# Optimization experiments

Measured on AMD Instinct MI355X. Metric: run time of the kernel, lower is better.

The kernel has to match this reference:

```python
import jax, jax.numpy as jnp
import numpy as np

BETA, ALPHA, NS_STEPS = 0.9, 1.0, 1
D_MODEL, D_STATE, D_CONV, EXPAND = 768, 16, 4, 2
D_INNER = EXPAND * D_MODEL
DT_RANK = -(-D_MODEL // 16)  # ceil(d_model/16) = 48
B, L = 2, 1024


def setup_inputs() -> dict:
    key = jax.random.key(0)
    ks = jax.random.split(key, 8)
    s = lambda k, shape, sc=0.02: jax.random.normal(k, shape, jnp.float32) * sc
    return {
        "hidden_states": jax.random.normal(ks[0], (B, L, D_MODEL), jnp.float32),
        "in_proj_w": s(ks[1], (2 * D_INNER, D_MODEL)),
        "conv_w": s(ks[2], (D_INNER, 1, D_CONV), 0.2),
        "conv_b": jnp.zeros((D_INNER,), jnp.float32),
        "x_proj_w": s(ks[3], (DT_RANK + 2 * D_STATE, D_INNER)),
        "dt_head_w": s(ks[4], (D_INNER, DT_RANK)),
        "dt_head_b": s(ks[5], (D_INNER,), 0.1),
        "out_proj_w": s(ks[6], (D_MODEL, D_INNER)),
        "D": jnp.ones((D_INNER,), jnp.float32),
    }


def _newton_schulz(G, steps):
    """Muon-style quintic Newton-Schulz orthogonalization of (b, d, n) with d >= n."""
    a, b, c = 3.4445, -4.7750, 2.0315
    X = G / (jnp.linalg.norm(G, axis=(-2, -1), keepdims=True) + 1e-7)
    X = X.swapaxes(-2, -1)  # (b, n, d): rows <= cols
    for _ in range(steps):
        A = X @ X.swapaxes(-2, -1)       # (b, n, n) small Gram
        Bm = b * A + c * (A @ A)
        X = a * X + Bm @ X
    return X.swapaxes(-2, -1)            # back to (b, d, n)


def reference(hidden_states, in_proj_w, conv_w, conv_b, x_proj_w, dt_head_w, dt_head_b, out_proj_w, D):
    Bz, Lz, _ = hidden_states.shape
    dtype = hidden_states.dtype
    # input projection -> x, z  (B, L, d_inner) each
    xz = jnp.einsum('bld,ed->ble', hidden_states, in_proj_w)
    x, z = jnp.split(xz, 2, axis=-1)
    # causal depthwise conv over time + SiLU
    xc = jax.lax.conv_general_dilated(
        x.swapaxes(1, 2), conv_w, (1,), [(D_CONV - 1, 0)],
        dimension_numbers=('NCH', 'OIH', 'NCH'), feature_group_count=D_INNER)
    x = jax.nn.silu(xc.swapaxes(1, 2) + conv_b)  # (B, L, d_inner)
    # projections for dt / k / q
    x_dbl = jnp.einsum('bld,ed->ble', x, x_proj_w)
    dt_low, k, q = jnp.split(x_dbl, [DT_RANK, DT_RANK + D_STATE], axis=-1)
    dt = jnp.einsum('blr,dr->bld', dt_low, dt_head_w)  # (B, L, d_inner), bias applied in scan

    def step(carry, inp):
        v, h = carry  # velocity / hidden states, each (b, d_inner, d_state)
        x_t, dt_t, k_t, q_t = inp
        dt_t = jax.nn.sigmoid(dt_t + dt_head_b)                              # (b, d)
        dt_t = dt_t / (1.0 + dt_t * jnp.sum(k_t * k_t, axis=-1, keepdims=True))
        dA = 1.0 - dt_t[:, :, None] * (k_t * k_t)[:, None, :]                # (b, d, n)
        G = (dt_t * x_t)[:, :, None] * k_t[:, None, :]                       # dt * u * k
        v = BETA * v + ALPHA * _newton_schulz(G, NS_STEPS)
        h = dA * h + v
        y_t = jnp.einsum('bdn,bn->bd', h, q_t) + D * x_t
        return (v, h), y_t

    init = (jnp.zeros((Bz, D_INNER, D_STATE), dtype),
            jnp.zeros((Bz, D_INNER, D_STATE), dtype))
    xs = (x.swapaxes(0, 1), dt.swapaxes(0, 1), k.swapaxes(0, 1), q.swapaxes(0, 1))
    _, y = jax.lax.scan(step, init, xs)        # (L, B, d_inner)
    y = y.swapaxes(0, 1) * jax.nn.silu(z)      # gate
    return jnp.einsum('bld,od->blo', y, out_proj_w)
```

## Files before the change

kernel.cpp:

```cpp
#include <hip/hip_runtime.h>

#define D_MODEL 768
#define D_STATE 16
#define D_INNER 1536
#define DT_RANK 48
#define NB 2
#define LSEQ 1024
#define NROWS (NB * LSEQ)
#define CCH 8
#define CLEN (LSEQ / CCH)
#define BETA_CL 1.3900845e-06f

typedef __attribute__((ext_vector_type(4))) float f32x4;
typedef __attribute__((ext_vector_type(8))) short s16x8;
typedef __attribute__((ext_vector_type(8))) unsigned short u16x8;

__device__ __forceinline__ unsigned short f2bu(float f) {
  unsigned int x = __builtin_bit_cast(unsigned int, f);
  x += 0x7fffu + ((x >> 16) & 1u);
  return (unsigned short)(x >> 16);
}

#define CVT_TOTAL 663552
#define Z1_GROUPS 20480
#define Z2_GROUPS 196608
__global__ __launch_bounds__(256) void cvt5z_kernel(const float* __restrict__ s0,
                                                    const float* __restrict__ s1,
                                                    const float* __restrict__ s2,
                                                    const float* __restrict__ s3,
                                                    const float* __restrict__ s4,
                                                    unsigned short* __restrict__ d0,
                                                    unsigned short* __restrict__ d1,
                                                    unsigned short* __restrict__ d2,
                                                    unsigned short* __restrict__ d3,
                                                    unsigned short* __restrict__ d4,
                                                    float* __restrict__ z1,
                                                    float* __restrict__ z2) {
  int g = blockIdx.x * 256 + threadIdx.x;
  if (g >= CVT_TOTAL) {
    int zg = g - CVT_TOTAL;
    f32x4 zero = {0.f, 0.f, 0.f, 0.f};
    if (zg < Z1_GROUPS) {
      *(f32x4*)(z1 + zg * 8) = zero;
      *(f32x4*)(z1 + zg * 8 + 4) = zero;
    } else if (zg < Z1_GROUPS + Z2_GROUPS) {
      int i = (zg - Z1_GROUPS) * 8;
      *(f32x4*)(z2 + i) = zero;
      *(f32x4*)(z2 + i + 4) = zero;
    }
    return;
  }
  const float* s;
  unsigned short* d;
  int base;
  if (g < 196608)      { s = s0; d = d0; base = 0; }
  else if (g < 491520) { s = s1; d = d1; base = 196608; }
  else if (g < 506880) { s = s2; d = d2; base = 491520; }
  else if (g < 516096) { s = s3; d = d3; base = 506880; }
  else                 { s = s4; d = d4; base = 516096; }
  int i = (g - base) * 8;
  f32x4 a = *(const f32x4*)(s + i);
  f32x4 b = *(const f32x4*)(s + i + 4);
  u16x8 o;
#pragma unroll
  for (int j = 0; j < 4; j++) { o[j] = f2bu(a[j]); o[4 + j] = f2bu(b[j]); }
  *(u16x8*)(d + i) = o;
}

template <bool ATOMIC>
__global__ __launch_bounds__(256) void gemm128(const unsigned short* __restrict__ A,
                                               const unsigned short* __restrict__ B,
                                               float* __restrict__ C, int K,
                                               int lda, int ldb, int ldc, int kseg_len) {
  __shared__ __align__(16) unsigned short As[2][128][40];
  __shared__ __align__(16) unsigned short Bs[2][128][40];
  const int m0 = blockIdx.y * 128, n0 = blockIdx.x * 128;
  const int kbeg = blockIdx.z * kseg_len;
  const int kend = kbeg + kseg_len;
  const int t = threadIdx.x;
  const int wave = t >> 6, lane = t & 63;
  const int wm = wave >> 1, wn = wave & 1;
  const int quad = lane >> 4, l16 = lane & 15;
  const int arow = t >> 1, kh = (t & 1) * 16;
  const unsigned short* Ap = A + (size_t)(m0 + arow) * lda + kh;
  const unsigned short* Bp = B + (size_t)(n0 + arow) * ldb + kh;

  u16x8 ra0, ra1, rb0, rb1;
  auto pref = [&](int k0) {
    ra0 = *(const u16x8*)(Ap + k0);
    ra1 = *(const u16x8*)(Ap + k0 + 8);
    rb0 = *(const u16x8*)(Bp + k0);
    rb1 = *(const u16x8*)(Bp + k0 + 8);
  };
  auto tolds = [&](int bi) {
    *(u16x8*)&As[bi][arow][kh] = ra0;
    *(u16x8*)&As[bi][arow][kh + 8] = ra1;
    *(u16x8*)&Bs[bi][arow][kh] = rb0;
    *(u16x8*)&Bs[bi][arow][kh + 8] = rb1;
  };

  f32x4 acc[4][4] = {};
  pref(kbeg);
  tolds(0);
  __syncthreads();
  int buf = 0;
  for (int k0 = kbeg; k0 < kend; k0 += 32) {
    const bool more = (k0 + 32 < kend);
    if (more) pref(k0 + 32);
    s16x8 af[4], bf[4];
#pragma unroll
    for (int i = 0; i < 4; i++) {
      af[i] = *(const s16x8*)&As[buf][wm * 64 + i * 16 + l16][quad * 8];
      bf[i] = *(const s16x8*)&Bs[buf][wn * 64 + i * 16 + l16][quad * 8];
    }
#pragma unroll
    for (int mi = 0; mi < 4; mi++)
#pragma unroll
      for (int ni = 0; ni < 4; ni++)
        acc[mi][ni] = __builtin_amdgcn_mfma_f32_16x16x32_bf16(af[mi], bf[ni], acc[mi][ni], 0, 0, 0);
    if (more) tolds(buf ^ 1);
    __syncthreads();
    buf ^= 1;
  }
#pragma unroll
  for (int mi = 0; mi < 4; mi++)
#pragma unroll
    for (int ni = 0; ni < 4; ni++)
#pragma unroll
      for (int r = 0; r < 4; r++) {
        int row = m0 + wm * 64 + mi * 16 + quad * 4 + r;
        int col = n0 + wn * 64 + ni * 16 + l16;
        if constexpr (ATOMIC)
          atomicAdd(&C[(size_t)row * ldc + col], acc[mi][ni][r]);
        else
          C[(size_t)row * ldc + col] = acc[mi][ni][r];
      }
}

template <bool AF32, bool ATOMIC>
__global__ __launch_bounds__(256) void gemm_bt(const void* __restrict__ Av,
                                               const unsigned short* __restrict__ B,
                                               float* __restrict__ C, int M, int N, int K,
                                               int lda, int ldb, int ldc, int kseg_len) {
  __shared__ __align__(16) unsigned short As[2][64][40];
  __shared__ __align__(16) unsigned short Bs[2][64][40];
  const int m0 = blockIdx.y * 64, n0 = blockIdx.x * 64;
  const int kbeg = blockIdx.z * kseg_len;
  const int kend = (kbeg + kseg_len < K) ? (kbeg + kseg_len) : K;
  const int t = threadIdx.x;
  const int wave = t >> 6, lane = t & 63;
  const int wm = wave >> 1, wn = wave & 1;
  const int quad = lane >> 4, l16 = lane & 15;
  const int srow = t >> 2;
  const int kseg = (t & 3) * 8;
  const bool va = (m0 + srow) < M, vb = (n0 + srow) < N;
  const float* Af = (const float*)Av;
  const unsigned short* Ab = (const unsigned short*)Av;
  const unsigned short* Bp = B + (size_t)(n0 + srow) * ldb;

  f32x4 ra0, ra1;
  u16x8 rab, rbb;
  auto pref = [&](int k0) {
    const int kk = k0 + kseg;
    const int krem = kend - kk;
    if constexpr (AF32) {
      const float* Ap = Af + (size_t)(m0 + srow) * lda + kk;
      if (va && krem >= 8) {
        ra0 = *(const f32x4*)Ap;
        ra1 = *(const f32x4*)(Ap + 4);
      } else {
#pragma unroll
        for (int j = 0; j < 4; j++) {
          ra0[j] = (va && j < krem) ? Ap[j] : 0.0f;
          ra1[j] = (va && j + 4 < krem) ? Ap[j + 4] : 0.0f;
        }
      }
    } else {
      const unsigned short* Ap = Ab + (size_t)(m0 + srow) * lda + kk;
      if (va && krem >= 8) {
        rab = *(const u16x8*)Ap;
      } else {
#pragma unroll
        for (int j = 0; j < 8; j++) rab[j] = (va && j < krem) ? Ap[j] : (unsigned short)0;
      }
    }
    if (vb && krem >= 8) {
      rbb = *(const u16x8*)(Bp + kk);
    } else {
#pragma unroll
      for (int j = 0; j < 8; j++) rbb[j] = (vb && j < krem) ? Bp[kk + j] : (unsigned short)0;
    }
  };
  auto tolds = [&](int bi) {
    if constexpr (AF32) {
      u16x8 oa;
#pragma unroll
      for (int j = 0; j < 4; j++) { oa[j] = f2bu(ra0[j]); oa[4 + j] = f2bu(ra1[j]); }
      *(u16x8*)&As[bi][srow][kseg] = oa;
    } else {
      *(u16x8*)&As[bi][srow][kseg] = rab;
    }
    *(u16x8*)&Bs[bi][srow][kseg] = rbb;
  };

  f32x4 acc[2][2] = {};
  pref(kbeg);
  tolds(0);
  __syncthreads();
  int buf = 0;
  for (int k0 = kbeg; k0 < kend; k0 += 32) {
    const bool more = (k0 + 32 < kend);
    if (more) pref(k0 + 32);
    s16x8 a0 = *(const s16x8*)&As[buf][wm * 32 + l16][quad * 8];
    s16x8 a1 = *(const s16x8*)&As[buf][wm * 32 + 16 + l16][quad * 8];
    s16x8 b0 = *(const s16x8*)&Bs[buf][wn * 32 + l16][quad * 8];
    s16x8 b1 = *(const s16x8*)&Bs[buf][wn * 32 + 16 + l16][quad * 8];
    acc[0][0] = __builtin_amdgcn_mfma_f32_16x16x32_bf16(a0, b0, acc[0][0], 0, 0, 0);
    acc[0][1] = __builtin_amdgcn_mfma_f32_16x16x32_bf16(a0, b1, acc[0][1], 0, 0, 0);
    acc[1][0] = __builtin_amdgcn_mfma_f32_16x16x32_bf16(a1, b0, acc[1][0], 0, 0, 0);
    acc[1][1] = __builtin_amdgcn_mfma_f32_16x16x32_bf16(a1, b1, acc[1][1], 0, 0, 0);
    if (more) tolds(buf ^ 1);
    __syncthreads();
    buf ^= 1;
  }
#pragma unroll
  for (int mi = 0; mi < 2; mi++)
#pragma unroll
    for (int ni = 0; ni < 2; ni++)
#pragma unroll
      for (int r = 0; r < 4; r++) {
        int row = m0 + wm * 32 + mi * 16 + quad * 4 + r;
        int col = n0 + wn * 32 + ni * 16 + l16;
        if (row < M && col < N) {
          if constexpr (ATOMIC)
            atomicAdd(&C[(size_t)row * ldc + col], acc[mi][ni][r]);
          else
            C[(size_t)row * ldc + col] = acc[mi][ni][r];
        }
      }
}

__global__ __launch_bounds__(256) void conv_silu_kernel(const float* __restrict__ xz,
                                                        const float* __restrict__ cw,
                                                        const float* __restrict__ cb,
                                                        float* __restrict__ xc,
                                                        unsigned short* __restrict__ xcb) {
  int idx = blockIdx.x * 256 + threadIdx.x;
  if (idx >= NROWS * D_INNER) return;
  int c = idx % D_INNER;
  int row = idx / D_INNER;
  int l = row & (LSEQ - 1);
  float acc = cb[c];
#pragma unroll
  for (int j = 0; j < 4; j++) {
    int dl = l - 3 + j;
    if (dl >= 0) acc += xz[(size_t)(row - 3 + j) * 3072 + c] * cw[c * 4 + j];
  }
  float sg = 1.0f / (1.0f + expf(-acc));
  float val = acc * sg;
  xc[idx] = val;
  xcb[idx] = f2bu(val);
}

__global__ __launch_bounds__(256) void precompute_kernel(const float* __restrict__ xdbl,
                                                         float* __restrict__ dtbuf,
                                                         const float* __restrict__ xconv,
                                                         const float* __restrict__ dtb,
                                                         float* __restrict__ ubuf,
                                                         float* __restrict__ kqbuf) {
  int row = blockIdx.x;
  int t = threadIdx.x;
  const float* xr = xdbl + (size_t)row * 80;
  float nk = 0.0f;
#pragma unroll
  for (int n = 0; n < 16; n++) { float kv = xr[48 + n]; nk += kv * kv; }
  float dtf[6], u0[6];
  float nupart = 0.0f;
#pragma unroll
  for (int i = 0; i < 6; i++) {
    int d = i * 256 + t;
    float draw = dtbuf[(size_t)row * D_INNER + d] + dtb[d];
    float sg = 1.0f / (1.0f + expf(-draw));
    float dv = sg / (1.0f + sg * nk);
    dtf[i] = dv;
    float u = dv * xconv[(size_t)row * D_INNER + d];
    u0[i] = u;
    nupart += u * u;
  }
  __shared__ float red[4];
  float v = nupart;
#pragma unroll
  for (int off = 32; off > 0; off >>= 1) v += __shfl_xor(v, off);
  if ((t & 63) == 0) red[t >> 6] = v;
  __syncthreads();
  float nu = red[0] + red[1] + red[2] + red[3];
  float p = nu * nk;
  float s = sqrtf(p) + 1e-7f;
  float tt = p / (s * s);
  float gamma = (3.4445f + tt * (-4.7750f + 2.0315f * tt)) / s;
#pragma unroll
  for (int i = 0; i < 6; i++) {
    int d = i * 256 + t;
    dtbuf[(size_t)row * D_INNER + d] = dtf[i];
    ubuf[(size_t)row * D_INNER + d] = gamma * u0[i];
  }
  if (t < 16) {
    kqbuf[(size_t)row * 32 + t] = xr[48 + t];
    kqbuf[(size_t)row * 32 + 16 + t] = xr[64 + t];
  }
}

__global__ __launch_bounds__(64) void scan_phase1(const float* __restrict__ ubuf,
                                                  const float* __restrict__ dtbuf,
                                                  const float* __restrict__ kqbuf,
                                                  float* __restrict__ cvp,
                                                  float* __restrict__ chp,
                                                  float* __restrict__ gp,
                                                  float* __restrict__ rp) {
  __shared__ float u_s[2][32][16];
  __shared__ float dt_s[2][32][16];
  __shared__ __align__(16) float kq_s[2][32][32];
  const int t = threadIdx.x;
  const int nq = t & 3, dloc = t >> 2;
  const int b = blockIdx.x / (96 * CCH);
  const int rem = blockIdx.x % (96 * CCH);
  const int d0 = (rem / CCH) * 16;
  const int c = rem % CCH;
  const int tbase = c * CLEN;
  const size_t ub = (size_t)b * LSEQ * D_INNER + d0;
  const float* kqb = kqbuf + (size_t)b * LSEQ * 32;
  const int scol = t & 15, srow0 = t >> 4;
  const int krow0 = t >> 3, kcol = (t & 7) * 4;
  float pu[8], pd[8];
  f32x4 pk[4];
  auto prefetch = [&](int t0) {
#pragma unroll
    for (int i = 0; i < 8; i++) {
      size_t off = ub + (size_t)(t0 + srow0 + 4 * i) * D_INNER + scol;
      pu[i] = ubuf[off];
      pd[i] = dtbuf[off];
    }
#pragma unroll
    for (int i = 0; i < 4; i++)
      pk[i] = *(const f32x4*)(kqb + (size_t)(t0 + krow0 + 8 * i) * 32 + kcol);
  };
  auto writelds = [&](int bi) {
#pragma unroll
    for (int i = 0; i < 8; i++) {
      u_s[bi][srow0 + 4 * i][scol] = pu[i];
      dt_s[bi][srow0 + 4 * i][scol] = pd[i];
    }
#pragma unroll
    for (int i = 0; i < 4; i++)
      *(f32x4*)&kq_s[bi][krow0 + 8 * i][kcol] = pk[i];
  };
  f32x4 v = {0.f, 0.f, 0.f, 0.f}, h = {0.f, 0.f, 0.f, 0.f};
  f32x4 g = {0.f, 0.f, 0.f, 0.f}, r = {1.f, 1.f, 1.f, 1.f};
  float bt = 0.9f;
  prefetch(tbase);
  writelds(0);
  int buf = 0;
  for (int t0 = 0; t0 < CLEN; t0 += 32) {
    const bool more = (t0 + 32 < CLEN);
    if (more) prefetch(tbase + t0 + 32);
#pragma unroll 4
    for (int s = 0; s < 32; s++) {
      float u = u_s[buf][s][dloc];
      float dtf = dt_s[buf][s][dloc];
      f32x4 kv = *(const f32x4*)&kq_s[buf][s][nq * 4];
#pragma unroll
      for (int j = 0; j < 4; j++) {
        float kj = kv[j];
        v[j] = fmaf(0.9f, v[j], u * kj);
        float a = fmaf(-dtf * kj, kj, 1.0f);
        h[j] = fmaf(a, h[j], v[j]);
        r[j] *= a;
        g[j] = fmaf(a, g[j], bt);
      }
      bt *= 0.9f;
    }
    if (more) writelds(buf ^ 1);
    buf ^= 1;
  }
  size_t o = (((size_t)b * CCH + c) * D_INNER + d0 + dloc) * 16 + nq * 4;
  *(f32x4*)(cvp + o) = v;
  *(f32x4*)(chp + o) = h;
  *(f32x4*)(gp + o) = g;
  *(f32x4*)(rp + o) = r;
}

__global__ __launch_bounds__(256) void scan_phase2(const float* __restrict__ cvp,
                                                   const float* __restrict__ chp,
                                                   float* __restrict__ gp,
                                                   float* __restrict__ rp) {
  int i = blockIdx.x * 256 + threadIdx.x;
  int b = i / (D_INNER * 16);
  int rem = i % (D_INNER * 16);
  float v0 = 0.f, h0 = 0.f;
#pragma unroll
  for (int c = 0; c < CCH; c++) {
    size_t o = ((size_t)(b * CCH + c)) * (D_INNER * 16) + rem;
    float cv = cvp[o], ch = chp[o], gg = gp[o], rr = rp[o];
    gp[o] = v0;
    rp[o] = h0;
    float v0n = fmaf(BETA_CL, v0, cv);
    float h0n = fmaf(gg, v0, fmaf(rr, h0, ch));
    v0 = v0n;
    h0 = h0n;
  }
}

__global__ __launch_bounds__(64) void scan_phase3(const float* __restrict__ ubuf,
                                                  const float* __restrict__ dtbuf,
                                                  const float* __restrict__ kqbuf,
                                                  const float* __restrict__ gp,
                                                  const float* __restrict__ rp,
                                                  float* __restrict__ ybuf) {
  __shared__ float u_s[2][32][16];
  __shared__ float dt_s[2][32][16];
  __shared__ __align__(16) float kq_s[2][32][32];
  const int t = threadIdx.x;
  const int nq = t & 3, dloc = t >> 2;
  const int b = blockIdx.x / (96 * CCH);
  const int rem = blockIdx.x % (96 * CCH);
  const int d0 = (rem / CCH) * 16;
  const int c = rem % CCH;
  const int tbase = c * CLEN;
  const size_t ub = (size_t)b * LSEQ * D_INNER + d0;
  const float* kqb = kqbuf + (size_t)b * LSEQ * 32;
  float* y_p = ybuf + (size_t)b * LSEQ * D_INNER + d0 + dloc;
  const int scol = t & 15, srow0 = t >> 4;
  const int krow0 = t >> 3, kcol = (t & 7) * 4;
  float pu[8], pd[8];
  f32x4 pk[4];
  auto prefetch = [&](int t0) {
#pragma unroll
    for (int i = 0; i < 8; i++) {
      size_t off = ub + (size_t)(t0 + srow0 + 4 * i) * D_INNER + scol;
      pu[i] = ubuf[off];
      pd[i] = dtbuf[off];
    }
#pragma unroll
    for (int i = 0; i < 4; i++)
      pk[i] = *(const f32x4*)(kqb + (size_t)(t0 + krow0 + 8 * i) * 32 + kcol);
  };
  auto writelds = [&](int bi) {
#pragma unroll
    for (int i = 0; i < 8; i++) {
      u_s[bi][srow0 + 4 * i][scol] = pu[i];
      dt_s[bi][srow0 + 4 * i][scol] = pd[i];
    }
#pragma unroll
    for (int i = 0; i < 4; i++)
      *(f32x4*)&kq_s[bi][krow0 + 8 * i][kcol] = pk[i];
  };
  size_t so = (((size_t)b * CCH + c) * D_INNER + d0 + dloc) * 16 + nq * 4;
  f32x4 v = *(const f32x4*)(gp + so);
  f32x4 h = *(const f32x4*)(rp + so);
  prefetch(tbase);
  writelds(0);
  int buf = 0;
  for (int t0 = 0; t0 < CLEN; t0 += 32) {
    const bool more = (t0 + 32 < CLEN);
    if (more) prefetch(tbase + t0 + 32);
#pragma unroll 4
    for (int s = 0; s < 32; s++) {
      float u = u_s[buf][s][dloc];
      float dtf = dt_s[buf][s][dloc];
      f32x4 kv = *(const f32x4*)&kq_s[buf][s][nq * 4];
      f32x4 qv = *(const f32x4*)&kq_s[buf][s][16 + nq * 4];
      float yp = 0.0f;
#pragma unroll
      for (int j = 0; j < 4; j++) {
        float kj = kv[j];
        v[j] = fmaf(0.9f, v[j], u * kj);
        float dA = fmaf(-dtf * kj, kj, 1.0f);
        h[j] = fmaf(dA, h[j], v[j]);
        yp = fmaf(h[j], qv[j], yp);
      }
      yp += __shfl_xor(yp, 1);
      yp += __shfl_xor(yp, 2);
      if (nq == 0) y_p[(size_t)(tbase + t0 + s) * D_INNER] = yp;
    }
    if (more) writelds(buf ^ 1);
    buf ^= 1;
  }
}

__global__ __launch_bounds__(256) void gate_kernel(const float* __restrict__ ybuf,
                                                   const float* __restrict__ xconv,
                                                   const float* __restrict__ xz,
                                                   const float* __restrict__ Dp,
                                                   unsigned short* __restrict__ ygb) {
  int idx = blockIdx.x * 256 + threadIdx.x;
  if (idx >= NROWS * D_INNER) return;
  int c = idx % D_INNER;
  int row = idx / D_INNER;
  float z = xz[(size_t)row * 3072 + 1536 + c];
  float sz = z / (1.0f + expf(-z));
  ygb[idx] = f2bu((ybuf[idx] + Dp[c] * xconv[idx]) * sz);
}

extern "C" void kernel_launch(void* const* d_in, const int* in_sizes, int n_in,
                              void* d_out, int out_size, void* d_ws, size_t ws_size,
                              hipStream_t stream) {
  const float* hidden = (const float*)d_in[0];
  const float* w_in   = (const float*)d_in[1];
  const float* conv_w = (const float*)d_in[2];
  const float* conv_b = (const float*)d_in[3];
  const float* w_x    = (const float*)d_in[4];
  const float* w_dt   = (const float*)d_in[5];
  const float* b_dt   = (const float*)d_in[6];
  const float* w_out  = (const float*)d_in[7];
  const float* Dp     = (const float*)d_in[8];

  float* ws    = (float*)d_ws;
  float* xz    = ws;
  float* xconv = xz + (size_t)NROWS * 3072;
  float* xdbl  = xconv + (size_t)NROWS * D_INNER;
  float* dtbuf = xdbl + (size_t)NROWS * 80;
  float* ubuf  = dtbuf + (size_t)NROWS * D_INNER;
  float* kqbuf = ubuf + (size_t)NROWS * D_INNER;
  float* ybuf  = kqbuf + (size_t)NROWS * 32;
  const size_t PL = (size_t)NB * CCH * D_INNER * 16;
  float* cvp   = ybuf + (size_t)NROWS * D_INNER;
  float* chp   = cvp + PL;
  float* gp    = chp + PL;
  float* rp    = gp + PL;
  unsigned short* bfr = (unsigned short*)(rp + PL);
  unsigned short* hbf = bfr;
  unsigned short* wib = hbf + 1572864;
  unsigned short* wxb = wib + 2359296;
  unsigned short* wdb = wxb + 122880;
  unsigned short* wob = wdb + 73728;
  unsigned short* xcb = wob + 1179648;
  unsigned short* ygb = xcb + 3145728;

  dim3 blk(256);
  cvt5z_kernel<<<dim3((CVT_TOTAL + Z1_GROUPS + Z2_GROUPS) / 256), blk, 0, stream>>>(
      hidden, w_in, w_x, w_dt, w_out, hbf, wib, wxb, wdb, wob, xdbl, (float*)d_out);
  gemm128<false><<<dim3(24, 16, 1), blk, 0, stream>>>(hbf, wib, xz, 768, 768, 768, 3072, 768);
  conv_silu_kernel<<<dim3(12288), blk, 0, stream>>>(xz, conv_w, conv_b, xconv, xcb);
  gemm_bt<false, true><<<dim3(2, 32, 8), blk, 0, stream>>>(xcb, wxb, xdbl, 2048, 80, 1536,
                                                           1536, 1536, 80, 192);
  gemm_bt<true, false><<<dim3(24, 32, 1), blk, 0, stream>>>(xdbl, wdb, dtbuf, 2048, 1536, 48,
                                                            80, 48, 1536, 48);
  precompute_kernel<<<dim3(NROWS), blk, 0, stream>>>(xdbl, dtbuf, xconv, b_dt, ubuf, kqbuf);
  scan_phase1<<<dim3(NB * 96 * CCH), dim3(64), 0, stream>>>(ubuf, dtbuf, kqbuf, cvp, chp, gp, rp);
  scan_phase2<<<dim3(192), blk, 0, stream>>>(cvp, chp, gp, rp);
  scan_phase3<<<dim3(NB * 96 * CCH), dim3(64), 0, stream>>>(ubuf, dtbuf, kqbuf, gp, rp, ybuf);
  gate_kernel<<<dim3(12288), blk, 0, stream>>>(ybuf, xconv, xz, Dp, ygb);
  gemm128<true><<<dim3(6, 16, 2), blk, 0, stream>>>(ygb, wob, (float*)d_out, 1536,
                                                    1536, 1536, 768, 768);
}
```

Baseline: 221.4 us.

## Fuse gate into scan phase3, use direct global-to-LDS loads in GEMM, split-K 4

The standalone gate kernel is folded into scan_phase3, which now stages xconv and z through shared memory and writes the gated bf16 output directly. This removes the fp32 y buffer round trip and one kernel launch. The GEMM staging switches from a register round trip to global_load_lds direct copies into an unpadded LDS layout, which may raise LDS bank conflicts on fragment reads. The out-projection split-K goes from 2 to 4 segments, adding more atomic adds to the output.

Result: slower. 229.7 us (+3.8%).

```diff
diff --git a/kernel.cpp b/kernel.cpp
--- a/kernel.cpp
+++ b/kernel.cpp
@@ -19,6 +19,12 @@
   unsigned int x = __builtin_bit_cast(unsigned int, f);
   x += 0x7fffu + ((x >> 16) & 1u);
   return (unsigned short)(x >> 16);
+}
+
+typedef __attribute__((address_space(3))) unsigned int as3u32;
+typedef __attribute__((address_space(1))) const unsigned int as1u32;
+__device__ __forceinline__ void gload16(const unsigned short* g, unsigned short* l) {
+  __builtin_amdgcn_global_load_lds((as1u32*)g, (as3u32*)l, 16, 0, 0);
 }
 
 #define CVT_TOTAL 663552
@@ -72,8 +78,8 @@
                                                const unsigned short* __restrict__ B,
                                                float* __restrict__ C, int K,
                                                int lda, int ldb, int ldc, int kseg_len) {
-  __shared__ __align__(16) unsigned short As[2][128][40];
-  __shared__ __align__(16) unsigned short Bs[2][128][40];
+  __shared__ __align__(16) unsigned short As[2][128 * 32];
+  __shared__ __align__(16) unsigned short Bs[2][128 * 32];
   const int m0 = blockIdx.y * 128, n0 = blockIdx.x * 128;
   const int kbeg = blockIdx.z * kseg_len;
   const int kend = kbeg + kseg_len;
@@ -81,44 +87,35 @@
   const int wave = t >> 6, lane = t & 63;
   const int wm = wave >> 1, wn = wave & 1;
   const int quad = lane >> 4, l16 = lane & 15;
-  const int arow = t >> 1, kh = (t & 1) * 16;
-  const unsigned short* Ap = A + (size_t)(m0 + arow) * lda + kh;
-  const unsigned short* Bp = B + (size_t)(n0 + arow) * ldb + kh;
-
-  u16x8 ra0, ra1, rb0, rb1;
-  auto pref = [&](int k0) {
-    ra0 = *(const u16x8*)(Ap + k0);
-    ra1 = *(const u16x8*)(Ap + k0 + 8);
-    rb0 = *(const u16x8*)(Bp + k0);
-    rb1 = *(const u16x8*)(Bp + k0 + 8);
-  };
-  auto tolds = [&](int bi) {
-    *(u16x8*)&As[bi][arow][kh] = ra0;
-    *(u16x8*)&As[bi][arow][kh + 8] = ra1;
-    *(u16x8*)&Bs[bi][arow][kh] = rb0;
-    *(u16x8*)&Bs[bi][arow][kh + 8] = rb1;
+  const int srow = lane >> 2;
+  const int kcol = (lane & 3) * 8;
+
+  auto stage = [&](int bi, int k0) {
+#pragma unroll
+    for (int r = 0; r < 2; r++) {
+      const int seg = r * 64 + wave * 16;
+      gload16(A + (size_t)(m0 + seg + srow) * lda + k0 + kcol, &As[bi][seg * 32]);
+      gload16(B + (size_t)(n0 + seg + srow) * ldb + k0 + kcol, &Bs[bi][seg * 32]);
+    }
   };
 
   f32x4 acc[4][4] = {};
-  pref(kbeg);
-  tolds(0);
+  stage(0, kbeg);
   __syncthreads();
   int buf = 0;
   for (int k0 = kbeg; k0 < kend; k0 += 32) {
-    const bool more = (k0 + 32 < kend);
-    if (more) pref(k0 + 32);
+    if (k0 + 32 < kend) stage(buf ^ 1, k0 + 32);
     s16x8 af[4], bf[4];
 #pragma unroll
     for (int i = 0; i < 4; i++) {
-      af[i] = *(const s16x8*)&As[buf][wm * 64 + i * 16 + l16][quad * 8];
-      bf[i] = *(const s16x8*)&Bs[buf][wn * 64 + i * 16 + l16][quad * 8];
+      af[i] = *(const s16x8*)&As[buf][(wm * 64 + i * 16 + l16) * 32 + quad * 8];
+      bf[i] = *(const s16x8*)&Bs[buf][(wn * 64 + i * 16 + l16) * 32 + quad * 8];
     }
 #pragma unroll
     for (int mi = 0; mi < 4; mi++)
 #pragma unroll
       for (int ni = 0; ni < 4; ni++)
         acc[mi][ni] = __builtin_amdgcn_mfma_f32_16x16x32_bf16(af[mi], bf[ni], acc[mi][ni], 0, 0, 0);
-    if (more) tolds(buf ^ 1);
     __syncthreads();
     buf ^= 1;
   }
@@ -415,10 +412,15 @@
                                                   const float* __restrict__ kqbuf,
                                                   const float* __restrict__ gp,
                                                   const float* __restrict__ rp,
-                                                  float* __restrict__ ybuf) {
+                                                  const float* __restrict__ xconv,
+                                                  const float* __restrict__ xz,
+                                                  const float* __restrict__ Dp,
+                                                  unsigned short* __restrict__ ygb) {
   __shared__ float u_s[2][32][16];
   __shared__ float dt_s[2][32][16];
   __shared__ __align__(16) float kq_s[2][32][32];
+  __shared__ float xc_s[2][32][16];
+  __shared__ float z_s[2][32][16];
   const int t = threadIdx.x;
   const int nq = t & 3, dloc = t >> 2;
   const int b = blockIdx.x / (96 * CCH);
@@ -428,10 +430,11 @@
   const int tbase = c * CLEN;
   const size_t ub = (size_t)b * LSEQ * D_INNER + d0;
   const float* kqb = kqbuf + (size_t)b * LSEQ * 32;
-  float* y_p = ybuf + (size_t)b * LSEQ * D_INNER + d0 + dloc;
+  const float* xzb = xz + (size_t)b * LSEQ * 3072 + 1536 + d0;
+  unsigned short* y_p = ygb + (size_t)b * LSEQ * D_INNER + d0 + dloc;
   const int scol = t & 15, srow0 = t >> 4;
   const int krow0 = t >> 3, kcol = (t & 7) * 4;
-  float pu[8], pd[8];
+  float pu[8], pd[8], pxc[8], pz[8];
   f32x4 pk[4];
   auto prefetch = [&](int t0) {
 #pragma unroll
@@ -439,6 +442,8 @@
       size_t off = ub + (size_t)(t0 + srow0 + 4 * i) * D_INNER + scol;
       pu[i] = ubuf[off];
       pd[i] = dtbuf[off];
+      pxc[i] = xconv[off];
+      pz[i] = xzb[(size_t)(t0 + srow0 + 4 * i) * 3072 + scol];
     }
 #pragma unroll
     for (int i = 0; i < 4; i++)
@@ -449,6 +454,8 @@
     for (int i = 0; i < 8; i++) {
       u_s[bi][srow0 + 4 * i][scol] = pu[i];
       dt_s[bi][srow0 + 4 * i][scol] = pd[i];
+      xc_s[bi][srow0 + 4 * i][scol] = pxc[i];
+      z_s[bi][srow0 + 4 * i][scol] = pz[i];
     }
 #pragma unroll
     for (int i = 0; i < 4; i++)
@@ -457,6 +464,7 @@
   size_t so = (((size_t)b * CCH + c) * D_INNER + d0 + dloc) * 16 + nq * 4;
   f32x4 v = *(const f32x4*)(gp + so);
   f32x4 h = *(const f32x4*)(rp + so);
+  const float Dd = Dp[d0 + dloc];
   prefetch(tbase);
   writelds(0);
   int buf = 0;
@@ -480,25 +488,14 @@
       }
       yp += __shfl_xor(yp, 1);
       yp += __shfl_xor(yp, 2);
-      if (nq == 0) y_p[(size_t)(tbase + t0 + s) * D_INNER] = yp;
+      float zv = z_s[buf][s][dloc];
+      float sz = zv / (1.0f + expf(-zv));
+      float val = (yp + Dd * xc_s[buf][s][dloc]) * sz;
+      if (nq == 0) y_p[(size_t)(tbase + t0 + s) * D_INNER] = f2bu(val);
     }
     if (more) writelds(buf ^ 1);
     buf ^= 1;
   }
-}
-
-__global__ __launch_bounds__(256) void gate_kernel(const float* __restrict__ ybuf,
-                                                   const float* __restrict__ xconv,
-                                                   const float* __restrict__ xz,
-                                                   const float* __restrict__ Dp,
-                                                   unsigned short* __restrict__ ygb) {
-  int idx = blockIdx.x * 256 + threadIdx.x;
-  if (idx >= NROWS * D_INNER) return;
-  int c = idx % D_INNER;
-  int row = idx / D_INNER;
-  float z = xz[(size_t)row * 3072 + 1536 + c];
-  float sz = z / (1.0f + expf(-z));
-  ygb[idx] = f2bu((ybuf[idx] + Dp[c] * xconv[idx]) * sz);
 }
 
 extern "C" void kernel_launch(void* const* d_in, const int* in_sizes, int n_in,
@@ -548,8 +545,8 @@
   precompute_kernel<<<dim3(NROWS), blk, 0, stream>>>(xdbl, dtbuf, xconv, b_dt, ubuf, kqbuf);
   scan_phase1<<<dim3(NB * 96 * CCH), dim3(64), 0, stream>>>(ubuf, dtbuf, kqbuf, cvp, chp, gp, rp);
   scan_phase2<<<dim3(192), blk, 0, stream>>>(cvp, chp, gp, rp);
-  scan_phase3<<<dim3(NB * 96 * CCH), dim3(64), 0, stream>>>(ubuf, dtbuf, kqbuf, gp, rp, ybuf);
-  gate_kernel<<<dim3(12288), blk, 0, stream>>>(ybuf, xconv, xz, Dp, ygb);
-  gemm128<true><<<dim3(6, 16, 2), blk, 0, stream>>>(ygb, wob, (float*)d_out, 1536,
-                                                    1536, 1536, 768, 768);
-}
+  scan_phase3<<<dim3(NB * 96 * CCH), dim3(64), 0, stream>>>(ubuf, dtbuf, kqbuf, gp, rp,
+                                                            xconv, xz, Dp, ygb);
+  gemm128<true><<<dim3(6, 16, 4), blk, 0, stream>>>(ygb, wob, (float*)d_out, 1536,
+                                                    1536, 1536, 768, 384);
+}
```
